# Kernel optimization log

Measured on AMD Instinct MI355X. Metric: run time of the kernel, lower is better.

Reference implementation:

```python
import jax, jax.numpy as jnp
import numpy as np

EPS = 1e-5
NEG_FILL = -1e20

B, C, N = 16, 256, 128
ALPHA = 2
CQK = C // ALPHA  # 128


def setup_inputs() -> dict:
    key = jax.random.key(0)
    k1, k2, k3, k4, k5 = jax.random.split(key, 5)
    x = jax.random.normal(k1, (B, C, N, N), dtype=jnp.float32)
    mask = jax.random.randint(k2, (B, N, N), 0, 2, dtype=jnp.int32)
    in_weight = 1.0 + 0.02 * jax.random.normal(k3, (C,), dtype=jnp.float32)
    in_bias = 0.02 * jax.random.normal(k4, (C,), dtype=jnp.float32)
    # 1x1 conv weight, no bias: out channels = 2*CQK + C = 512
    qkv_w = jax.random.normal(k5, (2 * CQK + C, C), dtype=jnp.float32) / jnp.sqrt(jnp.float32(C))
    return {"x": x, "mask": mask, "in_weight": in_weight, "in_bias": in_bias, "qkv_w": qkv_w}


def _forward(x, mask, in_weight, in_bias, qkv_w):
    b, c, h, w = x.shape
    # InstanceNorm2d(affine=True): per-sample, per-channel stats over (H, W)
    mu = jnp.mean(x, axis=(2, 3), keepdims=True)
    var = jnp.mean(jnp.square(x - mu), axis=(2, 3), keepdims=True)
    xn = (x - mu) * jax.lax.rsqrt(var + EPS)
    xn = xn * in_weight[None, :, None, None] + in_bias[None, :, None, None]
    # 1x1 conv == channel matmul
    qkv = jnp.einsum('oc,bchw->bohw', qkv_w, xn)
    cqk = c // ALPHA
    q, k, v = qkv[:, :cqk], qkv[:, cqk:2 * cqk], qkv[:, 2 * cqk:]
    # column (height-axis) attention energies: (b, h, w, h')
    energy_H = jnp.einsum('bchw,bcgw->bhwg', q, k)
    diag = jnp.eye(h, dtype=bool)[None, :, None, :]  # (1, h, 1, h')
    energy_H = jnp.where(diag, -jnp.inf, energy_H)
    # row (width-axis) attention energies: (b, h, w, w')
    energy_W = jnp.einsum('bchw,bchv->bhwv', q, k)
    energy = jnp.concatenate([energy_H, energy_W], axis=-1)  # (b, h, w, h+w)
    energy = jnp.where((mask == 0)[..., None], NEG_FILL, energy)
    att = jax.nn.softmax(energy, axis=-1)
    att_H, att_W = att[..., :h], att[..., h:]
    out_H = jnp.einsum('bcgw,bhwg->bchw', v, att_H)
    out_W = jnp.einsum('bchv,bhwv->bchw', v, att_W)
    return out_H + out_W + x, energy


def reference(x, mask, in_weight, in_bias, qkv_w):
    return _forward(x, mask, in_weight, in_bias, qkv_w)
```

## Files before the change

kernel.cpp:

```cpp
#include <hip/hip_runtime.h>
#include <math.h>

#define BB 16
#define CC_ 256
#define NS 128
#define OO 512
#define CQK 128
#define NN 16384
#define EPSV 1e-5f
#define NEG_FILL -1e20f

typedef _Float16 half8 __attribute__((ext_vector_type(8)));
typedef float floatx16 __attribute__((ext_vector_type(16)));

__global__ __launch_bounds__(256) void k_stats(const float* __restrict__ x,
                                               float* __restrict__ meanv,
                                               float* __restrict__ rstdv) {
    int bc = blockIdx.x;
    const float4* p4 = (const float4*)(x + (size_t)bc * NN);
    float s = 0.f, sq = 0.f;
    for (int i = threadIdx.x; i < NN / 4; i += 256) {
        float4 v = p4[i];
        s += (v.x + v.y) + (v.z + v.w);
        sq += v.x * v.x + v.y * v.y + v.z * v.z + v.w * v.w;
    }
    for (int off = 32; off > 0; off >>= 1) {
        s += __shfl_down(s, off);
        sq += __shfl_down(sq, off);
    }
    __shared__ float ss[4], ssq[4];
    int lane = threadIdx.x & 63, wid = threadIdx.x >> 6;
    if (lane == 0) { ss[wid] = s; ssq[wid] = sq; }
    __syncthreads();
    if (threadIdx.x == 0) {
        float st = ss[0] + ss[1] + ss[2] + ss[3];
        float sqt = ssq[0] + ssq[1] + ssq[2] + ssq[3];
        float mu = st * (1.f / NN);
        float var = sqt * (1.f / NN) - mu * mu;
        meanv[bc] = mu;
        rstdv[bc] = rsqrtf(var + EPSV);
    }
}

__global__ __launch_bounds__(256) void k_xsplit(const float* __restrict__ x,
                                                _Float16* __restrict__ xh,
                                                _Float16* __restrict__ xl) {
    __shared__ float tile[64][65];
    int b = blockIdx.z, c0 = blockIdx.y * 64, p0 = blockIdx.x * 64;
    int t = threadIdx.x;
    const float* src = x + ((size_t)b * CC_ + c0) * NN + p0;
#pragma unroll
    for (int i = 0; i < 4; i++) {
        int f = t + i * 256;
        int r = f >> 4, q = f & 15;
        float4 v = *(const float4*)(src + (size_t)r * NN + q * 4);
        tile[r][q * 4 + 0] = v.x; tile[r][q * 4 + 1] = v.y;
        tile[r][q * 4 + 2] = v.z; tile[r][q * 4 + 3] = v.w;
    }
    __syncthreads();
#pragma unroll
    for (int i = 0; i < 2; i++) {
        int f = t + i * 256;
        int pr = f >> 3, cq = f & 7;
        half8 h, l;
#pragma unroll
        for (int j = 0; j < 8; j++) {
            float v = tile[cq * 8 + j][pr];
            _Float16 hi = (_Float16)v;
            h[j] = hi;
            l[j] = (_Float16)(v - (float)hi);
        }
        size_t dst = ((size_t)b * NN + p0 + pr) * CC_ + c0 + cq * 8;
        *(half8*)(xh + dst) = h;
        *(half8*)(xl + dst) = l;
    }
}

__global__ __launch_bounds__(256) void k_weff(const float* __restrict__ qkv_w,
                                              const float* __restrict__ in_w,
                                              const float* __restrict__ in_b,
                                              const float* __restrict__ meanv,
                                              const float* __restrict__ rstdv,
                                              _Float16* __restrict__ wh,
                                              _Float16* __restrict__ wl,
                                              float* __restrict__ biasb) {
    int o = blockIdx.x, b = blockIdx.y, c = threadIdx.x;
    float w = qkv_w[o * CC_ + c];
    float s = rstdv[b * CC_ + c] * in_w[c];
    float t = in_b[c] - meanv[b * CC_ + c] * s;
    float wv = w * s * 16.f;
    _Float16 hi = (_Float16)wv;
    _Float16 lo = (_Float16)(wv - (float)hi);
    wh[((size_t)b * OO + o) * CC_ + c] = hi;
    wl[((size_t)b * OO + o) * CC_ + c] = lo;
    float part = w * t;
    for (int off = 32; off > 0; off >>= 1) part += __shfl_down(part, off);
    __shared__ float ps[4];
    int lane = c & 63, wid = c >> 6;
    if (lane == 0) ps[wid] = part;
    __syncthreads();
    if (c == 0) biasb[b * OO + o] = ps[0] + ps[1] + ps[2] + ps[3];
}

__global__ __launch_bounds__(512) void k_gemm(const _Float16* __restrict__ wh,
                                              const _Float16* __restrict__ wl,
                                              const _Float16* __restrict__ xh,
                                              const _Float16* __restrict__ xl,
                                              const float* __restrict__ biasb,
                                              float* __restrict__ qkv) {
    __shared__ _Float16 a_h[256][40], a_l[256][40];
    __shared__ _Float16 b_h[128][40], b_l[128][40];
    int b = blockIdx.z;
    int o0 = blockIdx.y * 256;
    int p0 = blockIdx.x * 128;
    int t = threadIdx.x;
    const _Float16* whb = wh + ((size_t)b * OO + o0) * CC_;
    const _Float16* wlb = wl + ((size_t)b * OO + o0) * CC_;
    const _Float16* xhb = xh + ((size_t)b * NN + p0) * CC_;
    const _Float16* xlb = xl + ((size_t)b * NN + p0) * CC_;
    floatx16 acc00 = {0}, acc01 = {0}, acc10 = {0}, acc11 = {0};
    int lane = t & 63, wv = t >> 6;
    int wo = (wv >> 1) * 64, wp = (wv & 1) * 64;
    int lr = lane & 31, lg = lane >> 5;

    int arow0 = t >> 2, acq = t & 3;
    half8 pa0h, pa0l, pa1h, pa1l, pb0h, pb0l;

#define LOADT(k0)                                                              \
    {                                                                          \
        pa0h = *(const half8*)(whb + (size_t)arow0 * CC_ + (k0) + acq * 8);    \
        pa0l = *(const half8*)(wlb + (size_t)arow0 * CC_ + (k0) + acq * 8);    \
        pa1h = *(const half8*)(whb + (size_t)(arow0 + 128) * CC_ + (k0) + acq * 8); \
        pa1l = *(const half8*)(wlb + (size_t)(arow0 + 128) * CC_ + (k0) + acq * 8); \
        pb0h = *(const half8*)(xhb + (size_t)arow0 * CC_ + (k0) + acq * 8);    \
        pb0l = *(const half8*)(xlb + (size_t)arow0 * CC_ + (k0) + acq * 8);    \
    }
#define STORET()                                                               \
    {                                                                          \
        *(half8*)&a_h[arow0][acq * 8] = pa0h;                                  \
        *(half8*)&a_l[arow0][acq * 8] = pa0l;                                  \
        *(half8*)&a_h[arow0 + 128][acq * 8] = pa1h;                            \
        *(half8*)&a_l[arow0 + 128][acq * 8] = pa1l;                            \
        *(half8*)&b_h[arow0][acq * 8] = pb0h;                                  \
        *(half8*)&b_l[arow0][acq * 8] = pb0l;                                  \
    }

    LOADT(0);
    STORET();
    for (int k0 = 0; k0 < CC_; k0 += 32) {
        __syncthreads();
        if (k0 + 32 < CC_) LOADT(k0 + 32);
#pragma unroll
        for (int kk = 0; kk < 32; kk += 16) {
            int ka = kk + lg * 8;
            half8 ah0 = *(const half8*)&a_h[wo + lr][ka];
            half8 ah1 = *(const half8*)&a_h[wo + 32 + lr][ka];
            half8 al0 = *(const half8*)&a_l[wo + lr][ka];
            half8 al1 = *(const half8*)&a_l[wo + 32 + lr][ka];
            half8 bh0 = *(const half8*)&b_h[wp + lr][ka];
            half8 bh1 = *(const half8*)&b_h[wp + 32 + lr][ka];
            half8 bl0 = *(const half8*)&b_l[wp + lr][ka];
            half8 bl1 = *(const half8*)&b_l[wp + 32 + lr][ka];
            acc00 = __builtin_amdgcn_mfma_f32_32x32x16_f16(ah0, bh0, acc00, 0, 0, 0);
            acc01 = __builtin_amdgcn_mfma_f32_32x32x16_f16(ah0, bh1, acc01, 0, 0, 0);
            acc10 = __builtin_amdgcn_mfma_f32_32x32x16_f16(ah1, bh0, acc10, 0, 0, 0);
            acc11 = __builtin_amdgcn_mfma_f32_32x32x16_f16(ah1, bh1, acc11, 0, 0, 0);
            acc00 = __builtin_amdgcn_mfma_f32_32x32x16_f16(ah0, bl0, acc00, 0, 0, 0);
            acc01 = __builtin_amdgcn_mfma_f32_32x32x16_f16(ah0, bl1, acc01, 0, 0, 0);
            acc10 = __builtin_amdgcn_mfma_f32_32x32x16_f16(ah1, bl0, acc10, 0, 0, 0);
            acc11 = __builtin_amdgcn_mfma_f32_32x32x16_f16(ah1, bl1, acc11, 0, 0, 0);
            acc00 = __builtin_amdgcn_mfma_f32_32x32x16_f16(al0, bh0, acc00, 0, 0, 0);
            acc01 = __builtin_amdgcn_mfma_f32_32x32x16_f16(al0, bh1, acc01, 0, 0, 0);
            acc10 = __builtin_amdgcn_mfma_f32_32x32x16_f16(al1, bh0, acc10, 0, 0, 0);
            acc11 = __builtin_amdgcn_mfma_f32_32x32x16_f16(al1, bh1, acc11, 0, 0, 0);
        }
        __syncthreads();
        if (k0 + 32 < CC_) STORET();
    }
#undef LOADT
#undef STORET
#pragma unroll
    for (int reg = 0; reg < 16; reg++) {
        int r = (reg & 3) + 8 * (reg >> 2) + 4 * lg;
        {
            int o = o0 + wo + r;
            float bias = biasb[b * OO + o];
            float* dst = qkv + ((size_t)b * OO + o) * NN + p0 + wp + lr;
            dst[0]  = acc00[reg] * 0.0625f + bias;
            dst[32] = acc01[reg] * 0.0625f + bias;
        }
        {
            int o = o0 + wo + 32 + r;
            float bias = biasb[b * OO + o];
            float* dst = qkv + ((size_t)b * OO + o) * NN + p0 + wp + lr;
            dst[0]  = acc10[reg] * 0.0625f + bias;
            dst[32] = acc11[reg] * 0.0625f + bias;
        }
    }
}

__global__ __launch_bounds__(256) void k_transp(const float* __restrict__ qkv,
                                                float* __restrict__ qkvT) {
    __shared__ float tile[32][33];
    int bo = blockIdx.y;
    int tw = blockIdx.x & 3, th = blockIdx.x >> 2;
    const float* src = qkv + (size_t)bo * NN;
    float* dst = qkvT + (size_t)bo * NN;
    int r = threadIdx.x >> 5, cc = threadIdx.x & 31;
    int h0 = th * 32, w0 = tw * 32;
#pragma unroll
    for (int i = 0; i < 4; i++)
        tile[r + 8 * i][cc] = src[(h0 + r + 8 * i) * NS + w0 + cc];
    __syncthreads();
#pragma unroll
    for (int i = 0; i < 4; i++)
        dst[(w0 + r + 8 * i) * NS + h0 + cc] = tile[cc][r + 8 * i];
}

__global__ __launch_bounds__(256) void k_energyH(const float* __restrict__ qkvT,
                                                 const int* __restrict__ mask,
                                                 float* __restrict__ energy) {
    __shared__ float qs[32][132];
    __shared__ float ks[32][132];
    int b = blockIdx.x >> 7, w = blockIdx.x & 127;
    int t = threadIdx.x, tx = t & 15, ty = t >> 4;
    float acc[8][8] = {};
    const float* qb = qkvT + (size_t)b * OO * NN;
    for (int ct = 0; ct < CQK; ct += 32) {
#pragma unroll
        for (int i = 0; i < 4; i++) {
            int f = t + i * 256;
            int r = f >> 5, cq = f & 31;
            float4 qv = *(const float4*)(qb + (size_t)(ct + r) * NN + w * NS + cq * 4);
            float4 kv = *(const float4*)(qb + (size_t)(CQK + ct + r) * NN + w * NS + cq * 4);
            *(float4*)&qs[r][cq * 4] = qv;
            *(float4*)&ks[r][cq * 4] = kv;
        }
        __syncthreads();
#pragma unroll
        for (int c = 0; c < 32; c++) {
            float4 q0 = *(float4*)&qs[c][ty * 8];
            float4 q1 = *(float4*)&qs[c][ty * 8 + 4];
            float4 k0 = *(float4*)&ks[c][tx * 8];
            float4 k1 = *(float4*)&ks[c][tx * 8 + 4];
            float qv[8] = {q0.x, q0.y, q0.z, q0.w, q1.x, q1.y, q1.z, q1.w};
            float kv[8] = {k0.x, k0.y, k0.z, k0.w, k1.x, k1.y, k1.z, k1.w};
#pragma unroll
            for (int i = 0; i < 8; i++)
#pragma unroll
                for (int j = 0; j < 8; j++)
                    acc[i][j] = fmaf(qv[i], kv[j], acc[i][j]);
        }
        __syncthreads();
    }
#pragma unroll
    for (int i = 0; i < 8; i++) {
        int h = ty * 8 + i;
        int m = mask[b * NN + h * NS + w];
        float* dst = energy + ((size_t)(b * NS + h) * NS + w) * 256 + tx * 8;
        float e[8];
#pragma unroll
        for (int j = 0; j < 8; j++) {
            int g = tx * 8 + j;
            float v = acc[i][j];
            if (g == h) v = NEG_FILL;
            if (m == 0) v = NEG_FILL;
            e[j] = v;
        }
        *(float4*)dst = make_float4(e[0], e[1], e[2], e[3]);
        *(float4*)(dst + 4) = make_float4(e[4], e[5], e[6], e[7]);
    }
}

__global__ __launch_bounds__(256) void k_energyW(const float* __restrict__ qkv,
                                                 const int* __restrict__ mask,
                                                 float* __restrict__ energy) {
    __shared__ float qs[32][132];
    __shared__ float ks[32][132];
    int b = blockIdx.x >> 7, h = blockIdx.x & 127;
    int t = threadIdx.x, tx = t & 15, ty = t >> 4;
    float acc[8][8] = {};
    const float* qb = qkv + (size_t)b * OO * NN;
    for (int ct = 0; ct < CQK; ct += 32) {
#pragma unroll
        for (int i = 0; i < 4; i++) {
            int f = t + i * 256;
            int r = f >> 5, cq = f & 31;
            float4 qv = *(const float4*)(qb + (size_t)(ct + r) * NN + h * NS + cq * 4);
            float4 kv = *(const float4*)(qb + (size_t)(CQK + ct + r) * NN + h * NS + cq * 4);
            *(float4*)&qs[r][cq * 4] = qv;
            *(float4*)&ks[r][cq * 4] = kv;
        }
        __syncthreads();
#pragma unroll
        for (int c = 0; c < 32; c++) {
            float4 q0 = *(float4*)&qs[c][ty * 8];
            float4 q1 = *(float4*)&qs[c][ty * 8 + 4];
            float4 k0 = *(float4*)&ks[c][tx * 8];
            float4 k1 = *(float4*)&ks[c][tx * 8 + 4];
            float qv[8] = {q0.x, q0.y, q0.z, q0.w, q1.x, q1.y, q1.z, q1.w};
            float kv[8] = {k0.x, k0.y, k0.z, k0.w, k1.x, k1.y, k1.z, k1.w};
#pragma unroll
            for (int i = 0; i < 8; i++)
#pragma unroll
                for (int j = 0; j < 8; j++)
                    acc[i][j] = fmaf(qv[i], kv[j], acc[i][j]);
        }
        __syncthreads();
    }
#pragma unroll
    for (int i = 0; i < 8; i++) {
        int w = ty * 8 + i;
        int m = mask[b * NN + h * NS + w];
        float* dst = energy + ((size_t)(b * NS + h) * NS + w) * 256 + 128 + tx * 8;
        float e[8];
#pragma unroll
        for (int j = 0; j < 8; j++) {
            float v = acc[i][j];
            if (m == 0) v = NEG_FILL;
            e[j] = v;
        }
        *(float4*)dst = make_float4(e[0], e[1], e[2], e[3]);
        *(float4*)(dst + 4) = make_float4(e[4], e[5], e[6], e[7]);
    }
}

__global__ __launch_bounds__(64) void k_softmax(const float* __restrict__ energy,
                                                float* __restrict__ attbase) {
    int row = blockIdx.x;
    int tid = threadIdx.x;
    float4 e = *((const float4*)(energy + (size_t)row * 256) + tid);
    float mx = fmaxf(fmaxf(e.x, e.y), fmaxf(e.z, e.w));
    for (int m = 32; m > 0; m >>= 1) mx = fmaxf(mx, __shfl_xor(mx, m));
    float x0 = expf(e.x - mx), x1 = expf(e.y - mx), x2 = expf(e.z - mx), x3 = expf(e.w - mx);
    float s = (x0 + x1) + (x2 + x3);
    for (int m = 32; m > 0; m >>= 1) s += __shfl_xor(s, m);
    float inv = 1.f / s;
    int b = row >> 14, rem = row & 16383;
    float* att = attbase + (size_t)b * (OO * NN) + (size_t)rem * 256 + tid * 4;
    *(float4*)att = make_float4(x0 * inv, x1 * inv, x2 * inv, x3 * inv);
}

__global__ __launch_bounds__(256) void k_outW(const float* __restrict__ qkv,
                                              const float* __restrict__ x,
                                              float* __restrict__ out) {
    __shared__ float vt[32][132];
    __shared__ float at[32][132];
    int cs = blockIdx.x, h = blockIdx.y, b = blockIdx.z;
    int t = threadIdx.x, tx = t & 15, ty = t >> 4;
    float acc[8][8] = {};
    const float* vbase = qkv + ((size_t)b * OO + CC_ + cs * 128) * NN + h * NS;
    const float* abase = qkv + (size_t)b * (OO * NN) + (size_t)h * NS * 256 + 128;
    for (int v0 = 0; v0 < 128; v0 += 32) {
#pragma unroll
        for (int i = 0; i < 4; i++) {
            int f = t + i * 256;
            int cl = f >> 3, vq = f & 7;
            float4 vv = *(const float4*)(vbase + (size_t)cl * NN + v0 + vq * 4);
            vt[vq * 4 + 0][cl] = vv.x; vt[vq * 4 + 1][cl] = vv.y;
            vt[vq * 4 + 2][cl] = vv.z; vt[vq * 4 + 3][cl] = vv.w;
            float4 av = *(const float4*)(abase + (size_t)cl * 256 + v0 + vq * 4);
            at[vq * 4 + 0][cl] = av.x; at[vq * 4 + 1][cl] = av.y;
            at[vq * 4 + 2][cl] = av.z; at[vq * 4 + 3][cl] = av.w;
        }
        __syncthreads();
#pragma unroll
        for (int v = 0; v < 32; v++) {
            float4 c0 = *(float4*)&vt[v][ty * 8];
            float4 c1 = *(float4*)&vt[v][ty * 8 + 4];
            float4 w0 = *(float4*)&at[v][tx * 8];
            float4 w1 = *(float4*)&at[v][tx * 8 + 4];
            float cv[8] = {c0.x, c0.y, c0.z, c0.w, c1.x, c1.y, c1.z, c1.w};
            float wv[8] = {w0.x, w0.y, w0.z, w0.w, w1.x, w1.y, w1.z, w1.w};
#pragma unroll
            for (int i = 0; i < 8; i++)
#pragma unroll
                for (int j = 0; j < 8; j++)
                    acc[i][j] = fmaf(cv[i], wv[j], acc[i][j]);
        }
        __syncthreads();
    }
#pragma unroll
    for (int i = 0; i < 8; i++) {
        int c = cs * 128 + ty * 8 + i;
        size_t base = ((size_t)b * CC_ + c) * NN + h * NS + tx * 8;
        float4 xa = *(const float4*)(x + base);
        float4 xb2 = *(const float4*)(x + base + 4);
        float4 v0 = {acc[i][0] + xa.x, acc[i][1] + xa.y, acc[i][2] + xa.z, acc[i][3] + xa.w};
        float4 v1 = {acc[i][4] + xb2.x, acc[i][5] + xb2.y, acc[i][6] + xb2.z, acc[i][7] + xb2.w};
        *(float4*)(out + base) = v0;
        *(float4*)(out + base + 4) = v1;
    }
}

__global__ __launch_bounds__(256) void k_outH(const float* __restrict__ qkvT,
                                              const float* __restrict__ attq,
                                              float* __restrict__ ohT) {
    __shared__ float vt[32][132];
    __shared__ float at[32][132];
    int cs = blockIdx.x, w = blockIdx.y, b = blockIdx.z;
    int t = threadIdx.x, tx = t & 15, ty = t >> 4;
    float acc[8][8] = {};
    const float* vbase = qkvT + ((size_t)b * OO + CC_ + cs * 128) * NN + w * NS;
    const float* abase = attq + (size_t)b * (OO * NN) + (size_t)w * 256;
    for (int g0 = 0; g0 < 128; g0 += 32) {
#pragma unroll
        for (int i = 0; i < 4; i++) {
            int f = t + i * 256;
            int cl = f >> 3, gq = f & 7;
            float4 vv = *(const float4*)(vbase + (size_t)cl * NN + g0 + gq * 4);
            vt[gq * 4 + 0][cl] = vv.x; vt[gq * 4 + 1][cl] = vv.y;
            vt[gq * 4 + 2][cl] = vv.z; vt[gq * 4 + 3][cl] = vv.w;
            float4 av = *(const float4*)(abase + (size_t)cl * 32768 + g0 + gq * 4);
            at[gq * 4 + 0][cl] = av.x; at[gq * 4 + 1][cl] = av.y;
            at[gq * 4 + 2][cl] = av.z; at[gq * 4 + 3][cl] = av.w;
        }
        __syncthreads();
#pragma unroll
        for (int g = 0; g < 32; g++) {
            float4 c0 = *(float4*)&vt[g][ty * 8];
            float4 c1 = *(float4*)&vt[g][ty * 8 + 4];
            float4 h0 = *(float4*)&at[g][tx * 8];
            float4 h1 = *(float4*)&at[g][tx * 8 + 4];
            float cv[8] = {c0.x, c0.y, c0.z, c0.w, c1.x, c1.y, c1.z, c1.w};
            float hv[8] = {h0.x, h0.y, h0.z, h0.w, h1.x, h1.y, h1.z, h1.w};
#pragma unroll
            for (int i = 0; i < 8; i++)
#pragma unroll
                for (int j = 0; j < 8; j++)
                    acc[i][j] = fmaf(cv[i], hv[j], acc[i][j]);
        }
        __syncthreads();
    }
#pragma unroll
    for (int i = 0; i < 8; i++) {
        int c = cs * 128 + ty * 8 + i;
        float* dst = ohT + (size_t)b * (OO * NN) + ((size_t)w * 256 + c) * 128 + tx * 8;
        *(float4*)dst = make_float4(acc[i][0], acc[i][1], acc[i][2], acc[i][3]);
        *(float4*)(dst + 4) = make_float4(acc[i][4], acc[i][5], acc[i][6], acc[i][7]);
    }
}

__global__ __launch_bounds__(256) void k_addT(const float* __restrict__ ohT,
                                              float* __restrict__ out) {
    __shared__ float tile[32][33];
    int bc = blockIdx.y;
    int b = bc >> 8, c = bc & 255;
    int tw = blockIdx.x & 3, th = blockIdx.x >> 2;
    const float* src = ohT + (size_t)b * (OO * NN) + (size_t)c * 128;
    int r = threadIdx.x >> 5, cc = threadIdx.x & 31;
    int h0 = th * 32, w0 = tw * 32;
#pragma unroll
    for (int i = 0; i < 4; i++)
        tile[r + 8 * i][cc] = src[(size_t)(w0 + r + 8 * i) * 32768 + h0 + cc];
    __syncthreads();
#pragma unroll
    for (int i = 0; i < 4; i++) {
        float* d = out + (size_t)bc * NN + (h0 + r + 8 * i) * NS + w0 + cc;
        *d += tile[cc][r + 8 * i];
    }
}

extern "C" void kernel_launch(void* const* d_in, const int* in_sizes, int n_in,
                              void* d_out, int out_size, void* d_ws, size_t ws_size,
                              hipStream_t stream) {
    const float* x = (const float*)d_in[0];
    const int* mask = (const int*)d_in[1];
    const float* in_w = (const float*)d_in[2];
    const float* in_b = (const float*)d_in[3];
    const float* qkv_w = (const float*)d_in[4];

    float* out = (float*)d_out;
    float* energy = out + (size_t)BB * CC_ * NN;

    float* ws = (float*)d_ws;
    float* qkv  = ws;
    float* qkvT = ws + (size_t)BB * OO * NN;
    float* weffr = qkvT + (size_t)BB * OO * NN;
    float* biasb = weffr + (size_t)BB * OO * CC_;
    float* meanv = biasb + BB * OO;
    float* rstdv = meanv + BB * CC_;
    _Float16* weff_h = (_Float16*)weffr;
    _Float16* weff_l = weff_h + (size_t)BB * OO * CC_;
    _Float16* x_hT = (_Float16*)qkvT;
    _Float16* x_lT = x_hT + (size_t)BB * NN * CC_;

    hipLaunchKernelGGL(k_stats, dim3(BB * CC_), dim3(256), 0, stream, x, meanv, rstdv);
    hipLaunchKernelGGL(k_xsplit, dim3(NN / 64, CC_ / 64, BB), dim3(256), 0, stream,
                       x, x_hT, x_lT);
    hipLaunchKernelGGL(k_weff, dim3(OO, BB), dim3(256), 0, stream,
                       qkv_w, in_w, in_b, meanv, rstdv, weff_h, weff_l, biasb);
    hipLaunchKernelGGL(k_gemm, dim3(NN / 128, OO / 256, BB), dim3(512), 0, stream,
                       weff_h, weff_l, x_hT, x_lT, biasb, qkv);
    hipLaunchKernelGGL(k_transp, dim3(16, BB * OO), dim3(256), 0, stream, qkv, qkvT);
    hipLaunchKernelGGL(k_energyH, dim3(BB * NS), dim3(256), 0, stream, qkvT, mask, energy);
    hipLaunchKernelGGL(k_energyW, dim3(BB * NS), dim3(256), 0, stream, qkv, mask, energy);
    hipLaunchKernelGGL(k_softmax, dim3(BB * NN), dim3(64), 0, stream, energy, qkv);
    hipLaunchKernelGGL(k_outW, dim3(2, NS, BB), dim3(256), 0, stream, qkv, x, out);
    hipLaunchKernelGGL(k_outH, dim3(2, NS, BB), dim3(256), 0, stream, qkvT, qkv, qkvT);
    hipLaunchKernelGGL(k_addT, dim3(16, BB * CC_), dim3(256), 0, stream, qkvT, out);
}
```

Measured before the change: 2.103 ms.

## Move attention energy and output GEMMs to split-fp16 MFMA

Replaces the scalar fp32 FMA loops in the energy and output kernels with MFMA 32x32x16 fp16 instructions, splitting each operand into high and low halves (three products) to keep near-fp32 accuracy. The output kernels now cover all 256 channels in one 512-thread block instead of two channel halves. The softmax packs four rows per 256-thread block. The cost is extra conversion work during shared-memory staging and less coalesced scalar epilogue stores, with some precision risk from the split-fp16 scheme.

```diff
diff --git a/kernel.cpp b/kernel.cpp
--- a/kernel.cpp
+++ b/kernel.cpp
@@ -11,7 +11,13 @@
 #define NEG_FILL -1e20f
 
 typedef _Float16 half8 __attribute__((ext_vector_type(8)));
+typedef _Float16 half4_t __attribute__((ext_vector_type(4)));
 typedef float floatx16 __attribute__((ext_vector_type(16)));
+
+#define MFMA3(ACC, AH, AL, BH, BL)                                              \
+    ACC = __builtin_amdgcn_mfma_f32_32x32x16_f16(AH, BH, ACC, 0, 0, 0);         \
+    ACC = __builtin_amdgcn_mfma_f32_32x32x16_f16(AH, BL, ACC, 0, 0, 0);         \
+    ACC = __builtin_amdgcn_mfma_f32_32x32x16_f16(AL, BH, ACC, 0, 0, 0);
 
 __global__ __launch_bounds__(256) void k_stats(const float* __restrict__ x,
                                                float* __restrict__ meanv,
@@ -161,18 +167,10 @@
             half8 bh1 = *(const half8*)&b_h[wp + 32 + lr][ka];
             half8 bl0 = *(const half8*)&b_l[wp + lr][ka];
             half8 bl1 = *(const half8*)&b_l[wp + 32 + lr][ka];
-            acc00 = __builtin_amdgcn_mfma_f32_32x32x16_f16(ah0, bh0, acc00, 0, 0, 0);
-            acc01 = __builtin_amdgcn_mfma_f32_32x32x16_f16(ah0, bh1, acc01, 0, 0, 0);
-            acc10 = __builtin_amdgcn_mfma_f32_32x32x16_f16(ah1, bh0, acc10, 0, 0, 0);
-            acc11 = __builtin_amdgcn_mfma_f32_32x32x16_f16(ah1, bh1, acc11, 0, 0, 0);
-            acc00 = __builtin_amdgcn_mfma_f32_32x32x16_f16(ah0, bl0, acc00, 0, 0, 0);
-            acc01 = __builtin_amdgcn_mfma_f32_32x32x16_f16(ah0, bl1, acc01, 0, 0, 0);
-            acc10 = __builtin_amdgcn_mfma_f32_32x32x16_f16(ah1, bl0, acc10, 0, 0, 0);
-            acc11 = __builtin_amdgcn_mfma_f32_32x32x16_f16(ah1, bl1, acc11, 0, 0, 0);
-            acc00 = __builtin_amdgcn_mfma_f32_32x32x16_f16(al0, bh0, acc00, 0, 0, 0);
-            acc01 = __builtin_amdgcn_mfma_f32_32x32x16_f16(al0, bh1, acc01, 0, 0, 0);
-            acc10 = __builtin_amdgcn_mfma_f32_32x32x16_f16(al1, bh0, acc10, 0, 0, 0);
-            acc11 = __builtin_amdgcn_mfma_f32_32x32x16_f16(al1, bh1, acc11, 0, 0, 0);
+            MFMA3(acc00, ah0, al0, bh0, bl0);
+            MFMA3(acc01, ah0, al0, bh1, bl1);
+            MFMA3(acc10, ah1, al1, bh0, bl0);
+            MFMA3(acc11, ah1, al1, bh1, bl1);
         }
         __syncthreads();
         if (k0 + 32 < CC_) STORET();
@@ -220,115 +218,155 @@
 __global__ __launch_bounds__(256) void k_energyH(const float* __restrict__ qkvT,
                                                  const int* __restrict__ mask,
                                                  float* __restrict__ energy) {
-    __shared__ float qs[32][132];
-    __shared__ float ks[32][132];
-    int b = blockIdx.x >> 7, w = blockIdx.x & 127;
-    int t = threadIdx.x, tx = t & 15, ty = t >> 4;
-    float acc[8][8] = {};
-    const float* qb = qkvT + (size_t)b * OO * NN;
+    __shared__ _Float16 a_h[128 * 40], a_l[128 * 40];
+    __shared__ _Float16 b_h[128 * 40], b_l[128 * 40];
+    int w = blockIdx.x, b = blockIdx.y;
+    int t = threadIdx.x;
+    const float* qb = qkvT + (size_t)b * OO * NN + w * NS;
+    const float* kb = qb + (size_t)CQK * NN;
+    floatx16 acc00 = {0}, acc01 = {0}, acc10 = {0}, acc11 = {0};
+    int lane = t & 63, wvv = t >> 6;
+    int wo = (wvv >> 1) * 64, wp = (wvv & 1) * 64;
+    int lr = lane & 31, lg = lane >> 5;
     for (int ct = 0; ct < CQK; ct += 32) {
+        __syncthreads();
 #pragma unroll
         for (int i = 0; i < 4; i++) {
             int f = t + i * 256;
-            int r = f >> 5, cq = f & 31;
-            float4 qv = *(const float4*)(qb + (size_t)(ct + r) * NN + w * NS + cq * 4);
-            float4 kv = *(const float4*)(qb + (size_t)(CQK + ct + r) * NN + w * NS + cq * 4);
-            *(float4*)&qs[r][cq * 4] = qv;
-            *(float4*)&ks[r][cq * 4] = kv;
-        }
-        __syncthreads();
-#pragma unroll
-        for (int c = 0; c < 32; c++) {
-            float4 q0 = *(float4*)&qs[c][ty * 8];
-            float4 q1 = *(float4*)&qs[c][ty * 8 + 4];
-            float4 k0 = *(float4*)&ks[c][tx * 8];
-            float4 k1 = *(float4*)&ks[c][tx * 8 + 4];
-            float qv[8] = {q0.x, q0.y, q0.z, q0.w, q1.x, q1.y, q1.z, q1.w};
-            float kv[8] = {k0.x, k0.y, k0.z, k0.w, k1.x, k1.y, k1.z, k1.w};
-#pragma unroll
-            for (int i = 0; i < 8; i++)
-#pragma unroll
-                for (int j = 0; j < 8; j++)
-                    acc[i][j] = fmaf(qv[i], kv[j], acc[i][j]);
-        }
-        __syncthreads();
-    }
-#pragma unroll
-    for (int i = 0; i < 8; i++) {
-        int h = ty * 8 + i;
-        int m = mask[b * NN + h * NS + w];
-        float* dst = energy + ((size_t)(b * NS + h) * NS + w) * 256 + tx * 8;
-        float e[8];
-#pragma unroll
-        for (int j = 0; j < 8; j++) {
-            int g = tx * 8 + j;
-            float v = acc[i][j];
-            if (g == h) v = NEG_FILL;
-            if (m == 0) v = NEG_FILL;
-            e[j] = v;
-        }
-        *(float4*)dst = make_float4(e[0], e[1], e[2], e[3]);
-        *(float4*)(dst + 4) = make_float4(e[4], e[5], e[6], e[7]);
+            int kc = f >> 5, mq = f & 31;
+            float4 qv = *(const float4*)(qb + (size_t)(ct + kc) * NN + mq * 4);
+            float4 kv = *(const float4*)(kb + (size_t)(ct + kc) * NN + mq * 4);
+            float qa[4] = {qv.x, qv.y, qv.z, qv.w};
+            float kk4[4] = {kv.x, kv.y, kv.z, kv.w};
+#pragma unroll
+            for (int j = 0; j < 4; j++) {
+                int m = mq * 4 + j;
+                int idx = m * 40 + (kc ^ (((m >> 2) & 3) << 3));
+                _Float16 hq = (_Float16)qa[j];
+                a_h[idx] = hq;
+                a_l[idx] = (_Float16)(qa[j] - (float)hq);
+                _Float16 hk = (_Float16)kk4[j];
+                b_h[idx] = hk;
+                b_l[idx] = (_Float16)(kk4[j] - (float)hk);
+            }
+        }
+        __syncthreads();
+#pragma unroll
+        for (int kk = 0; kk < 32; kk += 16) {
+            int ka = kk + lg * 8;
+            int ra0 = wo + lr, ra1 = wo + 32 + lr;
+            int rb0 = wp + lr, rb1 = wp + 32 + lr;
+            half8 ah0 = *(const half8*)&a_h[ra0 * 40 + (ka ^ (((ra0 >> 2) & 3) << 3))];
+            half8 ah1 = *(const half8*)&a_h[ra1 * 40 + (ka ^ (((ra1 >> 2) & 3) << 3))];
+            half8 al0 = *(const half8*)&a_l[ra0 * 40 + (ka ^ (((ra0 >> 2) & 3) << 3))];
+            half8 al1 = *(const half8*)&a_l[ra1 * 40 + (ka ^ (((ra1 >> 2) & 3) << 3))];
+            half8 bh0 = *(const half8*)&b_h[rb0 * 40 + (ka ^ (((rb0 >> 2) & 3) << 3))];
+            half8 bh1 = *(const half8*)&b_h[rb1 * 40 + (ka ^ (((rb1 >> 2) & 3) << 3))];
+            half8 bl0 = *(const half8*)&b_l[rb0 * 40 + (ka ^ (((rb0 >> 2) & 3) << 3))];
+            half8 bl1 = *(const half8*)&b_l[rb1 * 40 + (ka ^ (((rb1 >> 2) & 3) << 3))];
+            MFMA3(acc00, ah0, al0, bh0, bl0);
+            MFMA3(acc01, ah0, al0, bh1, bl1);
+            MFMA3(acc10, ah1, al1, bh0, bl0);
+            MFMA3(acc11, ah1, al1, bh1, bl1);
+        }
+    }
+#pragma unroll
+    for (int reg = 0; reg < 16; reg++) {
+        int r = (reg & 3) + 8 * (reg >> 2) + 4 * lg;
+        int g0 = wp + lr, g1 = wp + 32 + lr;
+#pragma unroll
+        for (int hf = 0; hf < 2; hf++) {
+            int hh = wo + hf * 32 + r;
+            float v0 = hf ? acc10[reg] : acc00[reg];
+            float v1 = hf ? acc11[reg] : acc01[reg];
+            int mv = mask[b * NN + hh * NS + w];
+            if (g0 == hh) v0 = NEG_FILL;
+            if (g1 == hh) v1 = NEG_FILL;
+            if (mv == 0) { v0 = NEG_FILL; v1 = NEG_FILL; }
+            float* dst = energy + ((size_t)(b * NS + hh) * NS + w) * 256;
+            dst[g0] = v0;
+            dst[g1] = v1;
+        }
     }
 }
 
 __global__ __launch_bounds__(256) void k_energyW(const float* __restrict__ qkv,
                                                  const int* __restrict__ mask,
                                                  float* __restrict__ energy) {
-    __shared__ float qs[32][132];
-    __shared__ float ks[32][132];
-    int b = blockIdx.x >> 7, h = blockIdx.x & 127;
-    int t = threadIdx.x, tx = t & 15, ty = t >> 4;
-    float acc[8][8] = {};
-    const float* qb = qkv + (size_t)b * OO * NN;
+    __shared__ _Float16 a_h[128 * 40], a_l[128 * 40];
+    __shared__ _Float16 b_h[128 * 40], b_l[128 * 40];
+    int h = blockIdx.x, b = blockIdx.y;
+    int t = threadIdx.x;
+    const float* qb = qkv + (size_t)b * OO * NN + h * NS;
+    const float* kb = qb + (size_t)CQK * NN;
+    floatx16 acc00 = {0}, acc01 = {0}, acc10 = {0}, acc11 = {0};
+    int lane = t & 63, wvv = t >> 6;
+    int wo = (wvv >> 1) * 64, wp = (wvv & 1) * 64;
+    int lr = lane & 31, lg = lane >> 5;
     for (int ct = 0; ct < CQK; ct += 32) {
+        __syncthreads();
 #pragma unroll
         for (int i = 0; i < 4; i++) {
             int f = t + i * 256;
-            int r = f >> 5, cq = f & 31;
-            float4 qv = *(const float4*)(qb + (size_t)(ct + r) * NN + h * NS + cq * 4);
-            float4 kv = *(const float4*)(qb + (size_t)(CQK + ct + r) * NN + h * NS + cq * 4);
-            *(float4*)&qs[r][cq * 4] = qv;
-            *(float4*)&ks[r][cq * 4] = kv;
-        }
-        __syncthreads();
-#pragma unroll
-        for (int c = 0; c < 32; c++) {
-            float4 q0 = *(float4*)&qs[c][ty * 8];
-            float4 q1 = *(float4*)&qs[c][ty * 8 + 4];
-            float4 k0 = *(float4*)&ks[c][tx * 8];
-            float4 k1 = *(float4*)&ks[c][tx * 8 + 4];
-            float qv[8] = {q0.x, q0.y, q0.z, q0.w, q1.x, q1.y, q1.z, q1.w};
-            float kv[8] = {k0.x, k0.y, k0.z, k0.w, k1.x, k1.y, k1.z, k1.w};
-#pragma unroll
-            for (int i = 0; i < 8; i++)
-#pragma unroll
-                for (int j = 0; j < 8; j++)
-                    acc[i][j] = fmaf(qv[i], kv[j], acc[i][j]);
-        }
-        __syncthreads();
-    }
-#pragma unroll
-    for (int i = 0; i < 8; i++) {
-        int w = ty * 8 + i;
-        int m = mask[b * NN + h * NS + w];
-        float* dst = energy + ((size_t)(b * NS + h) * NS + w) * 256 + 128 + tx * 8;
-        float e[8];
-#pragma unroll
-        for (int j = 0; j < 8; j++) {
-            float v = acc[i][j];
-            if (m == 0) v = NEG_FILL;
-            e[j] = v;
-        }
-        *(float4*)dst = make_float4(e[0], e[1], e[2], e[3]);
-        *(float4*)(dst + 4) = make_float4(e[4], e[5], e[6], e[7]);
-    }
-}
-
-__global__ __launch_bounds__(64) void k_softmax(const float* __restrict__ energy,
-                                                float* __restrict__ attbase) {
-    int row = blockIdx.x;
-    int tid = threadIdx.x;
+            int kc = f >> 5, mq = f & 31;
+            float4 qv = *(const float4*)(qb + (size_t)(ct + kc) * NN + mq * 4);
+            float4 kv = *(const float4*)(kb + (size_t)(ct + kc) * NN + mq * 4);
+            float qa[4] = {qv.x, qv.y, qv.z, qv.w};
+            float kk4[4] = {kv.x, kv.y, kv.z, kv.w};
+#pragma unroll
+            for (int j = 0; j < 4; j++) {
+                int m = mq * 4 + j;
+                int idx = m * 40 + (kc ^ (((m >> 2) & 3) << 3));
+                _Float16 hq = (_Float16)qa[j];
+                a_h[idx] = hq;
+                a_l[idx] = (_Float16)(qa[j] - (float)hq);
+                _Float16 hk = (_Float16)kk4[j];
+                b_h[idx] = hk;
+                b_l[idx] = (_Float16)(kk4[j] - (float)hk);
+            }
+        }
+        __syncthreads();
+#pragma unroll
+        for (int kk = 0; kk < 32; kk += 16) {
+            int ka = kk + lg * 8;
+            int ra0 = wo + lr, ra1 = wo + 32 + lr;
+            int rb0 = wp + lr, rb1 = wp + 32 + lr;
+            half8 ah0 = *(const half8*)&a_h[ra0 * 40 + (ka ^ (((ra0 >> 2) & 3) << 3))];
+            half8 ah1 = *(const half8*)&a_h[ra1 * 40 + (ka ^ (((ra1 >> 2) & 3) << 3))];
+            half8 al0 = *(const half8*)&a_l[ra0 * 40 + (ka ^ (((ra0 >> 2) & 3) << 3))];
+            half8 al1 = *(const half8*)&a_l[ra1 * 40 + (ka ^ (((ra1 >> 2) & 3) << 3))];
+            half8 bh0 = *(const half8*)&b_h[rb0 * 40 + (ka ^ (((rb0 >> 2) & 3) << 3))];
+            half8 bh1 = *(const half8*)&b_h[rb1 * 40 + (ka ^ (((rb1 >> 2) & 3) << 3))];
+            half8 bl0 = *(const half8*)&b_l[rb0 * 40 + (ka ^ (((rb0 >> 2) & 3) << 3))];
+            half8 bl1 = *(const half8*)&b_l[rb1 * 40 + (ka ^ (((rb1 >> 2) & 3) << 3))];
+            MFMA3(acc00, ah0, al0, bh0, bl0);
+            MFMA3(acc01, ah0, al0, bh1, bl1);
+            MFMA3(acc10, ah1, al1, bh0, bl0);
+            MFMA3(acc11, ah1, al1, bh1, bl1);
+        }
+    }
+#pragma unroll
+    for (int reg = 0; reg < 16; reg++) {
+        int r = (reg & 3) + 8 * (reg >> 2) + 4 * lg;
+        int v0c = wp + lr, v1c = wp + 32 + lr;
+#pragma unroll
+        for (int hf = 0; hf < 2; hf++) {
+            int ww = wo + hf * 32 + r;
+            float v0 = hf ? acc10[reg] : acc00[reg];
+            float v1 = hf ? acc11[reg] : acc01[reg];
+            int mv = mask[b * NN + h * NS + ww];
+            if (mv == 0) { v0 = NEG_FILL; v1 = NEG_FILL; }
+            float* dst = energy + ((size_t)(b * NS + h) * NS + ww) * 256 + 128;
+            dst[v0c] = v0;
+            dst[v1c] = v1;
+        }
+    }
+}
+
+__global__ __launch_bounds__(256) void k_softmax(const float* __restrict__ energy,
+                                                 float* __restrict__ attbase) {
+    int row = blockIdx.x * 4 + (threadIdx.x >> 6);
+    int tid = threadIdx.x & 63;
     float4 e = *((const float4*)(energy + (size_t)row * 256) + tid);
     float mx = fmaxf(fmaxf(e.x, e.y), fmaxf(e.z, e.w));
     for (int m = 32; m > 0; m >>= 1) mx = fmaxf(mx, __shfl_xor(mx, m));
@@ -341,103 +379,153 @@
     *(float4*)att = make_float4(x0 * inv, x1 * inv, x2 * inv, x3 * inv);
 }
 
-__global__ __launch_bounds__(256) void k_outW(const float* __restrict__ qkv,
+__global__ __launch_bounds__(512) void k_outW(const float* __restrict__ qkv,
                                               const float* __restrict__ x,
                                               float* __restrict__ out) {
-    __shared__ float vt[32][132];
-    __shared__ float at[32][132];
-    int cs = blockIdx.x, h = blockIdx.y, b = blockIdx.z;
-    int t = threadIdx.x, tx = t & 15, ty = t >> 4;
-    float acc[8][8] = {};
-    const float* vbase = qkv + ((size_t)b * OO + CC_ + cs * 128) * NN + h * NS;
+    __shared__ _Float16 a_h[256 * 40], a_l[256 * 40];
+    __shared__ _Float16 b_h[128 * 40], b_l[128 * 40];
+    int h = blockIdx.x, b = blockIdx.y;
+    int t = threadIdx.x;
+    const float* vbase = qkv + ((size_t)b * OO + CC_) * NN + h * NS;
     const float* abase = qkv + (size_t)b * (OO * NN) + (size_t)h * NS * 256 + 128;
-    for (int v0 = 0; v0 < 128; v0 += 32) {
+    floatx16 acc00 = {0}, acc01 = {0}, acc10 = {0}, acc11 = {0};
+    int lane = t & 63, wvv = t >> 6;
+    int wo = (wvv >> 1) * 64, wp = (wvv & 1) * 64;
+    int lr = lane & 31, lg = lane >> 5;
+    for (int ct = 0; ct < 128; ct += 32) {
+        __syncthreads();
 #pragma unroll
         for (int i = 0; i < 4; i++) {
-            int f = t + i * 256;
-            int cl = f >> 3, vq = f & 7;
-            float4 vv = *(const float4*)(vbase + (size_t)cl * NN + v0 + vq * 4);
-            vt[vq * 4 + 0][cl] = vv.x; vt[vq * 4 + 1][cl] = vv.y;
-            vt[vq * 4 + 2][cl] = vv.z; vt[vq * 4 + 3][cl] = vv.w;
-            float4 av = *(const float4*)(abase + (size_t)cl * 256 + v0 + vq * 4);
-            at[vq * 4 + 0][cl] = av.x; at[vq * 4 + 1][cl] = av.y;
-            at[vq * 4 + 2][cl] = av.z; at[vq * 4 + 3][cl] = av.w;
-        }
-        __syncthreads();
-#pragma unroll
-        for (int v = 0; v < 32; v++) {
-            float4 c0 = *(float4*)&vt[v][ty * 8];
-            float4 c1 = *(float4*)&vt[v][ty * 8 + 4];
-            float4 w0 = *(float4*)&at[v][tx * 8];
-            float4 w1 = *(float4*)&at[v][tx * 8 + 4];
-            float cv[8] = {c0.x, c0.y, c0.z, c0.w, c1.x, c1.y, c1.z, c1.w};
-            float wv[8] = {w0.x, w0.y, w0.z, w0.w, w1.x, w1.y, w1.z, w1.w};
-#pragma unroll
-            for (int i = 0; i < 8; i++)
-#pragma unroll
-                for (int j = 0; j < 8; j++)
-                    acc[i][j] = fmaf(cv[i], wv[j], acc[i][j]);
-        }
-        __syncthreads();
-    }
-#pragma unroll
-    for (int i = 0; i < 8; i++) {
-        int c = cs * 128 + ty * 8 + i;
-        size_t base = ((size_t)b * CC_ + c) * NN + h * NS + tx * 8;
-        float4 xa = *(const float4*)(x + base);
-        float4 xb2 = *(const float4*)(x + base + 4);
-        float4 v0 = {acc[i][0] + xa.x, acc[i][1] + xa.y, acc[i][2] + xa.z, acc[i][3] + xa.w};
-        float4 v1 = {acc[i][4] + xb2.x, acc[i][5] + xb2.y, acc[i][6] + xb2.z, acc[i][7] + xb2.w};
-        *(float4*)(out + base) = v0;
-        *(float4*)(out + base + 4) = v1;
-    }
-}
-
-__global__ __launch_bounds__(256) void k_outH(const float* __restrict__ qkvT,
+            int f = t + i * 512;
+            int c = f >> 3, vq = f & 7;
+            float4 vv = *(const float4*)(vbase + (size_t)c * NN + ct + vq * 4);
+            half4_t hh, ll;
+            hh[0] = (_Float16)vv.x; ll[0] = (_Float16)(vv.x - (float)hh[0]);
+            hh[1] = (_Float16)vv.y; ll[1] = (_Float16)(vv.y - (float)hh[1]);
+            hh[2] = (_Float16)vv.z; ll[2] = (_Float16)(vv.z - (float)hh[2]);
+            hh[3] = (_Float16)vv.w; ll[3] = (_Float16)(vv.w - (float)hh[3]);
+            *(half4_t*)&a_h[c * 40 + vq * 4] = hh;
+            *(half4_t*)&a_l[c * 40 + vq * 4] = ll;
+        }
+#pragma unroll
+        for (int i = 0; i < 2; i++) {
+            int f = t + i * 512;
+            int ww = f >> 3, vq = f & 7;
+            float4 av = *(const float4*)(abase + (size_t)ww * 256 + ct + vq * 4);
+            half4_t hh, ll;
+            hh[0] = (_Float16)av.x; ll[0] = (_Float16)(av.x - (float)hh[0]);
+            hh[1] = (_Float16)av.y; ll[1] = (_Float16)(av.y - (float)hh[1]);
+            hh[2] = (_Float16)av.z; ll[2] = (_Float16)(av.z - (float)hh[2]);
+            hh[3] = (_Float16)av.w; ll[3] = (_Float16)(av.w - (float)hh[3]);
+            *(half4_t*)&b_h[ww * 40 + vq * 4] = hh;
+            *(half4_t*)&b_l[ww * 40 + vq * 4] = ll;
+        }
+        __syncthreads();
+#pragma unroll
+        for (int kk = 0; kk < 32; kk += 16) {
+            int ka = kk + lg * 8;
+            half8 ah0 = *(const half8*)&a_h[(wo + lr) * 40 + ka];
+            half8 ah1 = *(const half8*)&a_h[(wo + 32 + lr) * 40 + ka];
+            half8 al0 = *(const half8*)&a_l[(wo + lr) * 40 + ka];
+            half8 al1 = *(const half8*)&a_l[(wo + 32 + lr) * 40 + ka];
+            half8 bh0 = *(const half8*)&b_h[(wp + lr) * 40 + ka];
+            half8 bh1 = *(const half8*)&b_h[(wp + 32 + lr) * 40 + ka];
+            half8 bl0 = *(const half8*)&b_l[(wp + lr) * 40 + ka];
+            half8 bl1 = *(const half8*)&b_l[(wp + 32 + lr) * 40 + ka];
+            MFMA3(acc00, ah0, al0, bh0, bl0);
+            MFMA3(acc01, ah0, al0, bh1, bl1);
+            MFMA3(acc10, ah1, al1, bh0, bl0);
+            MFMA3(acc11, ah1, al1, bh1, bl1);
+        }
+    }
+#pragma unroll
+    for (int reg = 0; reg < 16; reg++) {
+        int r = (reg & 3) + 8 * (reg >> 2) + 4 * lg;
+        int w0c = wp + lr, w1c = wp + 32 + lr;
+#pragma unroll
+        for (int hf = 0; hf < 2; hf++) {
+            int c = wo + hf * 32 + r;
+            float v0 = hf ? acc10[reg] : acc00[reg];
+            float v1 = hf ? acc11[reg] : acc01[reg];
+            size_t base = ((size_t)b * CC_ + c) * NN + h * NS;
+            out[base + w0c] = v0 + x[base + w0c];
+            out[base + w1c] = v1 + x[base + w1c];
+        }
+    }
+}
+
+__global__ __launch_bounds__(512) void k_outH(const float* __restrict__ qkvT,
                                               const float* __restrict__ attq,
                                               float* __restrict__ ohT) {
-    __shared__ float vt[32][132];
-    __shared__ float at[32][132];
-    int cs = blockIdx.x, w = blockIdx.y, b = blockIdx.z;
-    int t = threadIdx.x, tx = t & 15, ty = t >> 4;
-    float acc[8][8] = {};
-    const float* vbase = qkvT + ((size_t)b * OO + CC_ + cs * 128) * NN + w * NS;
+    __shared__ _Float16 a_h[256 * 40], a_l[256 * 40];
+    __shared__ _Float16 b_h[128 * 40], b_l[128 * 40];
+    int w = blockIdx.x, b = blockIdx.y;
+    int t = threadIdx.x;
+    const float* vbase = qkvT + ((size_t)b * OO + CC_) * NN + w * NS;
     const float* abase = attq + (size_t)b * (OO * NN) + (size_t)w * 256;
-    for (int g0 = 0; g0 < 128; g0 += 32) {
+    floatx16 acc00 = {0}, acc01 = {0}, acc10 = {0}, acc11 = {0};
+    int lane = t & 63, wvv = t >> 6;
+    int wo = (wvv >> 1) * 64, wp = (wvv & 1) * 64;
+    int lr = lane & 31, lg = lane >> 5;
+    for (int ct = 0; ct < 128; ct += 32) {
+        __syncthreads();
 #pragma unroll
         for (int i = 0; i < 4; i++) {
-            int f = t + i * 256;
-            int cl = f >> 3, gq = f & 7;
-            float4 vv = *(const float4*)(vbase + (size_t)cl * NN + g0 + gq * 4);
-            vt[gq * 4 + 0][cl] = vv.x; vt[gq * 4 + 1][cl] = vv.y;
-            vt[gq * 4 + 2][cl] = vv.z; vt[gq * 4 + 3][cl] = vv.w;
-            float4 av = *(const float4*)(abase + (size_t)cl * 32768 + g0 + gq * 4);
-            at[gq * 4 + 0][cl] = av.x; at[gq * 4 + 1][cl] = av.y;
-            at[gq * 4 + 2][cl] = av.z; at[gq * 4 + 3][cl] = av.w;
-        }
-        __syncthreads();
-#pragma unroll
-        for (int g = 0; g < 32; g++) {
-            float4 c0 = *(float4*)&vt[g][ty * 8];
-            float4 c1 = *(float4*)&vt[g][ty * 8 + 4];
-            float4 h0 = *(float4*)&at[g][tx * 8];
-            float4 h1 = *(float4*)&at[g][tx * 8 + 4];
-            float cv[8] = {c0.x, c0.y, c0.z, c0.w, c1.x, c1.y, c1.z, c1.w};
-            float hv[8] = {h0.x, h0.y, h0.z, h0.w, h1.x, h1.y, h1.z, h1.w};
-#pragma unroll
-            for (int i = 0; i < 8; i++)
-#pragma unroll
-                for (int j = 0; j < 8; j++)
-                    acc[i][j] = fmaf(cv[i], hv[j], acc[i][j]);
-        }
-        __syncthreads();
-    }
-#pragma unroll
-    for (int i = 0; i < 8; i++) {
-        int c = cs * 128 + ty * 8 + i;
-        float* dst = ohT + (size_t)b * (OO * NN) + ((size_t)w * 256 + c) * 128 + tx * 8;
-        *(float4*)dst = make_float4(acc[i][0], acc[i][1], acc[i][2], acc[i][3]);
-        *(float4*)(dst + 4) = make_float4(acc[i][4], acc[i][5], acc[i][6], acc[i][7]);
+            int f = t + i * 512;
+            int c = f >> 3, gq = f & 7;
+            float4 vv = *(const float4*)(vbase + (size_t)c * NN + ct + gq * 4);
+            half4_t hh, ll;
+            hh[0] = (_Float16)vv.x; ll[0] = (_Float16)(vv.x - (float)hh[0]);
+            hh[1] = (_Float16)vv.y; ll[1] = (_Float16)(vv.y - (float)hh[1]);
+            hh[2] = (_Float16)vv.z; ll[2] = (_Float16)(vv.z - (float)hh[2]);
+            hh[3] = (_Float16)vv.w; ll[3] = (_Float16)(vv.w - (float)hh[3]);
+            *(half4_t*)&a_h[c * 40 + gq * 4] = hh;
+            *(half4_t*)&a_l[c * 40 + gq * 4] = ll;
+        }
+#pragma unroll
+        for (int i = 0; i < 2; i++) {
+            int f = t + i * 512;
+            int hh2 = f >> 3, gq = f & 7;
+            float4 av = *(const float4*)(abase + (size_t)hh2 * 32768 + ct + gq * 4);
+            half4_t hh, ll;
+            hh[0] = (_Float16)av.x; ll[0] = (_Float16)(av.x - (float)hh[0]);
+            hh[1] = (_Float16)av.y; ll[1] = (_Float16)(av.y - (float)hh[1]);
+            hh[2] = (_Float16)av.z; ll[2] = (_Float16)(av.z - (float)hh[2]);
+            hh[3] = (_Float16)av.w; ll[3] = (_Float16)(av.w - (float)hh[3]);
+            *(half4_t*)&b_h[hh2 * 40 + gq * 4] = hh;
+            *(half4_t*)&b_l[hh2 * 40 + gq * 4] = ll;
+        }
+        __syncthreads();
+#pragma unroll
+        for (int kk = 0; kk < 32; kk += 16) {
+            int ka = kk + lg * 8;
+            half8 ah0 = *(const half8*)&a_h[(wo + lr) * 40 + ka];
+            half8 ah1 = *(const half8*)&a_h[(wo + 32 + lr) * 40 + ka];
+            half8 al0 = *(const half8*)&a_l[(wo + lr) * 40 + ka];
+            half8 al1 = *(const half8*)&a_l[(wo + 32 + lr) * 40 + ka];
+            half8 bh0 = *(const half8*)&b_h[(wp + lr) * 40 + ka];
+            half8 bh1 = *(const half8*)&b_h[(wp + 32 + lr) * 40 + ka];
+            half8 bl0 = *(const half8*)&b_l[(wp + lr) * 40 + ka];
+            half8 bl1 = *(const half8*)&b_l[(wp + 32 + lr) * 40 + ka];
+            MFMA3(acc00, ah0, al0, bh0, bl0);
+            MFMA3(acc01, ah0, al0, bh1, bl1);
+            MFMA3(acc10, ah1, al1, bh0, bl0);
+            MFMA3(acc11, ah1, al1, bh1, bl1);
+        }
+    }
+#pragma unroll
+    for (int reg = 0; reg < 16; reg++) {
+        int r = (reg & 3) + 8 * (reg >> 2) + 4 * lg;
+        int h0c = wp + lr, h1c = wp + 32 + lr;
+#pragma unroll
+        for (int hf = 0; hf < 2; hf++) {
+            int c = wo + hf * 32 + r;
+            float v0 = hf ? acc10[reg] : acc00[reg];
+            float v1 = hf ? acc11[reg] : acc01[reg];
+            float* dst = ohT + (size_t)b * (OO * NN) + ((size_t)w * 256 + c) * 128;
+            dst[h0c] = v0;
+            dst[h1c] = v1;
+        }
     }
 }
 
@@ -493,10 +581,10 @@
     hipLaunchKernelGGL(k_gemm, dim3(NN / 128, OO / 256, BB), dim3(512), 0, stream,
                        weff_h, weff_l, x_hT, x_lT, biasb, qkv);
     hipLaunchKernelGGL(k_transp, dim3(16, BB * OO), dim3(256), 0, stream, qkv, qkvT);
-    hipLaunchKernelGGL(k_energyH, dim3(BB * NS), dim3(256), 0, stream, qkvT, mask, energy);
-    hipLaunchKernelGGL(k_energyW, dim3(BB * NS), dim3(256), 0, stream, qkv, mask, energy);
-    hipLaunchKernelGGL(k_softmax, dim3(BB * NN), dim3(64), 0, stream, energy, qkv);
-    hipLaunchKernelGGL(k_outW, dim3(2, NS, BB), dim3(256), 0, stream, qkv, x, out);
-    hipLaunchKernelGGL(k_outH, dim3(2, NS, BB), dim3(256), 0, stream, qkvT, qkv, qkvT);
+    hipLaunchKernelGGL(k_energyH, dim3(NS, BB), dim3(256), 0, stream, qkvT, mask, energy);
+    hipLaunchKernelGGL(k_energyW, dim3(NS, BB), dim3(256), 0, stream, qkv, mask, energy);
+    hipLaunchKernelGGL(k_softmax, dim3(BB * NN / 4), dim3(256), 0, stream, energy, qkv);
+    hipLaunchKernelGGL(k_outW, dim3(NS, BB), dim3(512), 0, stream, qkv, x, out);
+    hipLaunchKernelGGL(k_outH, dim3(NS, BB), dim3(512), 0, stream, qkvT, qkv, qkvT);
     hipLaunchKernelGGL(k_addT, dim3(16, BB * CC_), dim3(256), 0, stream, qkvT, out);
 }
```

Result: faster. 1.983 ms (-5.7%).
